# Kernel tuning notes

Hardware: AMD Instinct MI355X
Metric: run time of the kernel (lower is better)

The kernel has to match this reference:

```python
import jax, jax.numpy as jnp
import numpy as np

B, S, D, H, E = 2, 2048, 1024, 4096, 8


def setup_inputs() -> dict:
    key = jax.random.key(0)
    ks = jax.random.split(key, 8)
    sc = lambda *shape: 0.02
    x = jax.random.normal(ks[0], (B, S, D), dtype=jnp.float32)
    gate_w = jax.random.normal(ks[1], (D, E), dtype=jnp.float32) * 0.02
    gate_b = jnp.zeros((E,), dtype=jnp.float32)
    w1 = jax.random.normal(ks[2], (E, D, H), dtype=jnp.float32) * 0.02
    b1 = jnp.zeros((E, H), dtype=jnp.float32)
    w2 = jax.random.normal(ks[3], (E, H, D), dtype=jnp.float32) * 0.02
    b2 = jnp.zeros((E, D), dtype=jnp.float32)
    return {"x": x, "gate_w": gate_w, "gate_b": gate_b,
            "w1": w1, "b1": b1, "w2": w2, "b2": b2}


def reference(x, gate_w, gate_b, w1, b1, w2, b2):
    b, s, d = x.shape
    e = w1.shape[0]
    xf = x.reshape(-1, d)                       # [N, D]
    scores = xf @ gate_w + gate_b               # [N, E]
    # original does topk(k=2) but only uses topk_indices[:, 0] == argmax
    sel = jnp.argmax(scores, axis=-1)           # [N]
    out = jnp.zeros_like(xf)
    for ei in range(e):                         # small fixed expert loop
        h = jax.nn.gelu(xf @ w1[ei] + b1[ei], approximate=False)
        y = h @ w2[ei] + b2[ei]
        out = out + jnp.where((sel == ei)[:, None], y, jnp.zeros((), x.dtype))
    out = out.reshape(b, s, d)
    l_aux = jnp.zeros((), dtype=x.dtype)
    return out, l_aux
```

## Files before the change

### kernel.cpp

```cpp
#include <hip/hip_runtime.h>
#include <math.h>

#define NTOK 4096
#define DDIM 1024
#define HDIM 4096
#define NEXP 8
#define BK 64
#define T0MAX 40
#define T1MAX 72

typedef float f32x4 __attribute__((ext_vector_type(4)));
typedef __bf16 bf16x8 __attribute__((ext_vector_type(8)));
typedef const __attribute__((address_space(1))) void gas_t;
typedef __attribute__((address_space(3))) void las_t;

__device__ __forceinline__ unsigned short f2bf(float f) {
    union { float f; unsigned u; } v; v.f = f;
    unsigned u = v.u;
    return (unsigned short)((u + 0x7fffu + ((u >> 16) & 1u)) >> 16);
}

__device__ __forceinline__ float gelu_f(float v) {
    return 0.5f * v * (1.0f + erff(v * 0.70710678118654752f));
}

__global__ void k_gate(const float* __restrict__ x, const float* __restrict__ gw,
                       const float* __restrict__ gb, unsigned short* __restrict__ xb,
                       int* __restrict__ sel, int* __restrict__ counts) {
    const int wid = threadIdx.x >> 6, lane = threadIdx.x & 63;
    const int tok = blockIdx.x * 4 + wid;
    const float* xr = x + (long)tok * DDIM;
    unsigned short* xbr = xb + (long)tok * DDIM;
    float s[NEXP];
#pragma unroll
    for (int e = 0; e < NEXP; ++e) s[e] = 0.f;
    for (int it = 0; it < DDIM / 64; ++it) {
        const int kk = it * 64 + lane;
        const float xv = xr[kk];
        xbr[kk] = f2bf(xv);
        const float4* g4 = (const float4*)(gw + (long)kk * NEXP);
        const float4 g0 = g4[0], g1 = g4[1];
        s[0] += xv * g0.x; s[1] += xv * g0.y; s[2] += xv * g0.z; s[3] += xv * g0.w;
        s[4] += xv * g1.x; s[5] += xv * g1.y; s[6] += xv * g1.z; s[7] += xv * g1.w;
    }
#pragma unroll
    for (int e = 0; e < NEXP; ++e)
        for (int off = 32; off > 0; off >>= 1)
            s[e] += __shfl_down(s[e], off);
    if (lane == 0) {
        float best = s[0] + gb[0]; int bi = 0;
#pragma unroll
        for (int e = 1; e < NEXP; ++e) {
            const float v = s[e] + gb[e];
            if (v > best) { best = v; bi = e; }
        }
        sel[tok] = bi;
        atomicAdd(&counts[bi], 1);
    }
}

__global__ void k_fill(const int* __restrict__ sel, const int* __restrict__ counts,
                       int* __restrict__ cur, int* __restrict__ offs,
                       int* __restrict__ list, int* __restrict__ t0,
                       int* __restrict__ t1, float* __restrict__ laux) {
    const int t = blockIdx.x * blockDim.x + threadIdx.x;
    if (t < NTOK) {
        const int e = sel[t];
        int off_e = 0;
#pragma unroll
        for (int j = 0; j < NEXP; ++j) off_e += (j < e) ? counts[j] : 0;
        list[off_e + atomicAdd(&cur[e], 1)] = t;
    }
    if (t == 0) {
        int o = 0;
        for (int e = 0; e < NEXP; ++e) { offs[e] = o; o += counts[e]; }
        offs[NEXP] = o;
        int i0 = 0;
        for (int e = 0; e < NEXP; ++e)
            for (int m = 0; m < counts[e]; m += 128) t0[i0++] = (e << 16) | m;
        while (i0 < T0MAX) t0[i0++] = -1;
        int i1 = 0;
        for (int e = 0; e < NEXP; ++e)
            for (int m = 0; m < counts[e]; m += 64) t1[i1++] = (e << 16) | m;
        while (i1 < T1MAX) t1[i1++] = -1;
        laux[0] = 0.f;
    }
}

template<int K, int NC>
__global__ __launch_bounds__(256) void k_cvt_w(const float* __restrict__ W,
                                               unsigned short* __restrict__ Wt) {
    __shared__ unsigned short T[64 * 68];
    const int ktiles = K / 64;
    const int e  = blockIdx.y / ktiles;
    const int k0 = (blockIdx.y % ktiles) * 64;
    const int n0 = blockIdx.x * 64;
    const float* src = W + (long)e * K * NC + (long)k0 * NC + n0;
    const int tid = threadIdx.x;
#pragma unroll
    for (int i = 0; i < 4; ++i) {
        const int idx = tid + i * 256;
        const int k = idx >> 4, c4 = (idx & 15) * 4;
        const float4 v = *(const float4*)(src + (long)k * NC + c4);
        T[(c4 + 0) * 68 + k] = f2bf(v.x);
        T[(c4 + 1) * 68 + k] = f2bf(v.y);
        T[(c4 + 2) * 68 + k] = f2bf(v.z);
        T[(c4 + 3) * 68 + k] = f2bf(v.w);
    }
    __syncthreads();
    unsigned short* dst = Wt + (long)e * NC * K + (long)n0 * K + k0;
#pragma unroll
    for (int i = 0; i < 2; ++i) {
        const int idx = tid + i * 256;
        const int n = idx >> 3, c8 = (idx & 7) * 8;
        *(ushort4*)(dst + (long)n * K + c8)     = *(const ushort4*)&T[n * 68 + c8];
        *(ushort4*)(dst + (long)n * K + c8 + 4) = *(const ushort4*)&T[n * 68 + c8 + 4];
    }
}

template<int MODE, int BM_, int BN_>
__global__ __launch_bounds__(256) void k_gemm(
        const unsigned short* __restrict__ Ain,
        const unsigned short* __restrict__ Wt,
        const float* __restrict__ bias,
        unsigned short* __restrict__ Hout, float* __restrict__ Yout,
        const int* __restrict__ counts, const int* __restrict__ offs,
        const int* __restrict__ list, const int* __restrict__ ttab) {
    static_assert(BM_ % 32 == 0 && BN_ % 32 == 0, "tile");
    constexpr int K  = (MODE == 0) ? DDIM : HDIM;
    constexpr int NC = (MODE == 0) ? HDIM : DDIM;
    constexpr int NT = K / BK;
    constexpr int FM = BM_ / 32;
    constexpr int FN = BN_ / 32;
    constexpr int LA = BM_ / 32;
    constexpr int LB = BN_ / 32;
    constexpr int EP = 136;
    constexpr int STAGE_SH = BM_ * 64 + BN_ * 64;
    constexpr int SH_SZ = (MODE == 0 && BM_ * EP > STAGE_SH) ? BM_ * EP : STAGE_SH;

    const int code = ttab[blockIdx.y];
    if (code < 0) return;
    const int e  = code >> 16;
    const int m0 = code & 0xFFFF;
    const int cnt  = counts[e];
    const int base = offs[e];
    const int n0   = blockIdx.x * BN_;

    __shared__ __align__(16) unsigned short sh[SH_SZ];
    unsigned short* Asb = sh;
    unsigned short* Btb = sh + BM_ * 64;

    const int tid  = threadIdx.x;
    const int lane = tid & 63, wid = tid >> 6;
    const int lr = lane >> 3, lc = lane & 7;
    const int sb = (lc * 16) ^ (lr << 4);

    const unsigned short* pA[LA];
#pragma unroll
    for (int i = 0; i < LA; ++i) {
        const int r = wid * (BM_ / 4) + i * 8 + lr;
        int rr = m0 + r; if (rr >= cnt) rr = cnt - 1;
        const long grow = (MODE == 0) ? (long)list[base + rr] : (long)(base + rr);
        pA[i] = (const unsigned short*)((const char*)(Ain + grow * K) + sb);
    }
    const unsigned short* We = Wt + (long)e * NC * K;
    const unsigned short* pB[LB];
#pragma unroll
    for (int i = 0; i < LB; ++i) {
        const int r = wid * (BN_ / 4) + i * 8 + lr;
        pB[i] = (const unsigned short*)((const char*)(We + (long)(n0 + r) * K) + sb);
    }

    const int wm = (wid >> 1) * (BM_ / 2);
    const int wn = (wid & 1) * 64;
    const int hk = 16 * (lane >> 4);

    const f32x4 zero4 = {0.f, 0.f, 0.f, 0.f};
    f32x4 acc[FM][FN];
#pragma unroll
    for (int i = 0; i < FM; ++i)
#pragma unroll
        for (int j = 0; j < FN; ++j) acc[i][j] = zero4;

    for (int t = 0; t < NT; ++t) {
        __syncthreads();
#pragma unroll
        for (int i = 0; i < LA; ++i)
            __builtin_amdgcn_global_load_lds((gas_t*)(pA[i] + t * 64),
                (las_t*)(Asb + (wid * (BM_ / 4) + i * 8) * 64), 16, 0, 0);
#pragma unroll
        for (int i = 0; i < LB; ++i)
            __builtin_amdgcn_global_load_lds((gas_t*)(pB[i] + t * 64),
                (las_t*)(Btb + (wid * (BN_ / 4) + i * 8) * 64), 16, 0, 0);
        __syncthreads();
#pragma unroll
        for (int kk = 0; kk < BK; kk += 32) {
            bf16x8 a[FM], b[FN];
#pragma unroll
            for (int mf = 0; mf < FM; ++mf) {
                const int r  = wm + mf * 16 + (lane & 15);
                const int kb = (2 * kk + hk) ^ ((r & 7) << 4);
                a[mf] = *(const bf16x8*)((const char*)Asb + r * 128 + kb);
            }
#pragma unroll
            for (int nf = 0; nf < FN; ++nf) {
                const int cc = wn + nf * 16 + (lane & 15);
                const int kb = (2 * kk + hk) ^ ((cc & 7) << 4);
                b[nf] = *(const bf16x8*)((const char*)Btb + cc * 128 + kb);
            }
            __builtin_amdgcn_s_setprio(1);
#pragma unroll
            for (int mf = 0; mf < FM; ++mf)
#pragma unroll
                for (int nf = 0; nf < FN; ++nf)
                    acc[mf][nf] = __builtin_amdgcn_mfma_f32_16x16x32_bf16(
                        a[mf], b[nf], acc[mf][nf], 0, 0, 0);
            __builtin_amdgcn_s_setprio(0);
        }
    }

    if constexpr (MODE == 0) {
        __syncthreads();
#pragma unroll
        for (int nf = 0; nf < FN; ++nf) {
            const int cl = wn + nf * 16 + (lane & 15);
            const float bv = bias[(long)e * NC + n0 + cl];
#pragma unroll
            for (int mf = 0; mf < FM; ++mf) {
#pragma unroll
                for (int ri = 0; ri < 4; ++ri) {
                    const int rl = wm + mf * 16 + (lane >> 4) * 4 + ri;
                    sh[rl * EP + cl] = f2bf(gelu_f(acc[mf][nf][ri] + bv));
                }
            }
        }
        __syncthreads();
        const int row = tid >> 1, ch = (tid & 1) * 64;
        if (m0 + row < cnt) {
            char* dst = (char*)(Hout + (long)(base + m0 + row) * HDIM + n0 + ch);
            const char* srcp = (const char*)sh + row * (EP * 2) + ch * 2;
#pragma unroll
            for (int j = 0; j < 4; ++j) {
                const int4 v0 = *(const int4*)(srcp + j * 32);
                const int4 v1 = *(const int4*)(srcp + j * 32 + 16);
                *(int4*)(dst + j * 32)      = v0;
                *(int4*)(dst + j * 32 + 16) = v1;
            }
        }
    } else {
#pragma unroll
        for (int nf = 0; nf < FN; ++nf) {
            const int coln = n0 + wn + nf * 16 + (lane & 15);
            const float bv = bias[(long)e * NC + coln];
#pragma unroll
            for (int mf = 0; mf < FM; ++mf) {
                const int rb = m0 + wm + mf * 16 + (lane >> 4) * 4;
#pragma unroll
                for (int ri = 0; ri < 4; ++ri) {
                    const int row = rb + ri;
                    if (row < cnt)
                        Yout[(long)list[base + row] * DDIM + coln] = acc[mf][nf][ri] + bv;
                }
            }
        }
    }
}

extern "C" void kernel_launch(void* const* d_in, const int* in_sizes, int n_in,
                              void* d_out, int out_size, void* d_ws, size_t ws_size,
                              hipStream_t stream) {
    const float* x      = (const float*)d_in[0];
    const float* gate_w = (const float*)d_in[1];
    const float* gate_b = (const float*)d_in[2];
    const float* w1     = (const float*)d_in[3];
    const float* b1     = (const float*)d_in[4];
    const float* w2     = (const float*)d_in[5];
    const float* b2     = (const float*)d_in[6];
    float* out = (float*)d_out;

    char* ws = (char*)d_ws;
    int* counts  = (int*)(ws);
    int* cur     = (int*)(ws + 128);
    int* offs    = (int*)(ws + 256);
    int* t0      = (int*)(ws + 512);
    int* t1      = (int*)(ws + 768);
    int* sel     = (int*)(ws + 4096);
    int* list    = (int*)(ws + 20480);
    unsigned short* xb  = (unsigned short*)(ws + 65536);
    unsigned short* Hws = (unsigned short*)(ws + 65536 + 8388608);
    unsigned short* Wtb = (unsigned short*)(ws + 65536 + 8388608 + 33554432);
    const size_t WS_NEEDED = 65536 + 8388608 + 33554432 + 67108864;
    if (ws_size < WS_NEEDED) return;

    hipMemsetAsync(ws, 0, 256, stream);
    k_gate<<<NTOK / 4, 256, 0, stream>>>(x, gate_w, gate_b, xb, sel, counts);
    k_fill<<<(NTOK + 255) / 256, 256, 0, stream>>>(sel, counts, cur, offs, list, t0, t1,
                                                   out + (long)NTOK * DDIM);

    k_cvt_w<DDIM, HDIM><<<dim3(HDIM / 64, NEXP * (DDIM / 64)), 256, 0, stream>>>(w1, Wtb);
    k_gemm<0, 128, 128><<<dim3(HDIM / 128, T0MAX), 256, 0, stream>>>(
        xb, Wtb, b1, Hws, nullptr, counts, offs, list, t0);

    k_cvt_w<HDIM, DDIM><<<dim3(DDIM / 64, NEXP * (HDIM / 64)), 256, 0, stream>>>(w2, Wtb);
    k_gemm<1, 64, 128><<<dim3(DDIM / 128, T1MAX), 256, 0, stream>>>(
        Hws, Wtb, b2, nullptr, out, counts, offs, list, t1);
}
```

Before: 279.8 us.

## Shrink GEMM LDS footprint with two-pass epilogue and smaller second-GEMM tile

The first GEMM's epilogue now stages its GELU output through LDS in two 64-row halves, so shared memory is only as large as the staging buffers rather than BM*136. This lowers LDS use per block and may allow more resident blocks per CU, at the cost of an extra barrier pass. The second GEMM moves from a 64x128 tile to a 64x64 tile, doubling the column-block grid, and the warp column offset is generalised to BN/2 so the smaller tile works.

New measurement: 291.1 us. 1.04x slower.

```diff
diff --git a/kernel.cpp b/kernel.cpp
--- a/kernel.cpp
+++ b/kernel.cpp
@@ -135,8 +135,6 @@
     constexpr int LA = BM_ / 32;
     constexpr int LB = BN_ / 32;
     constexpr int EP = 136;
-    constexpr int STAGE_SH = BM_ * 64 + BN_ * 64;
-    constexpr int SH_SZ = (MODE == 0 && BM_ * EP > STAGE_SH) ? BM_ * EP : STAGE_SH;
 
     const int code = ttab[blockIdx.y];
     if (code < 0) return;
@@ -146,7 +144,7 @@
     const int base = offs[e];
     const int n0   = blockIdx.x * BN_;
 
-    __shared__ __align__(16) unsigned short sh[SH_SZ];
+    __shared__ __align__(16) unsigned short sh[BM_ * 64 + BN_ * 64];
     unsigned short* Asb = sh;
     unsigned short* Btb = sh + BM_ * 64;
 
@@ -172,7 +170,7 @@
     }
 
     const int wm = (wid >> 1) * (BM_ / 2);
-    const int wn = (wid & 1) * 64;
+    const int wn = (wid & 1) * (BN_ / 2);
     const int hk = 16 * (lane >> 4);
 
     const f32x4 zero4 = {0.f, 0.f, 0.f, 0.f};
@@ -220,31 +218,36 @@
     }
 
     if constexpr (MODE == 0) {
-        __syncthreads();
-#pragma unroll
-        for (int nf = 0; nf < FN; ++nf) {
-            const int cl = wn + nf * 16 + (lane & 15);
-            const float bv = bias[(long)e * NC + n0 + cl];
-#pragma unroll
-            for (int mf = 0; mf < FM; ++mf) {
-#pragma unroll
-                for (int ri = 0; ri < 4; ++ri) {
-                    const int rl = wm + mf * 16 + (lane >> 4) * 4 + ri;
-                    sh[rl * EP + cl] = f2bf(gelu_f(acc[mf][nf][ri] + bv));
+        float bvv[FN];
+#pragma unroll
+        for (int nf = 0; nf < FN; ++nf)
+            bvv[nf] = bias[(long)e * NC + n0 + wn + nf * 16 + (lane & 15)];
+#pragma unroll
+        for (int p = 0; p < 2; ++p) {
+            __syncthreads();
+            if ((wid >> 1) == p) {
+#pragma unroll
+                for (int nf = 0; nf < FN; ++nf) {
+                    const int cl = wn + nf * 16 + (lane & 15);
+#pragma unroll
+                    for (int mf = 0; mf < FM; ++mf) {
+#pragma unroll
+                        for (int ri = 0; ri < 4; ++ri) {
+                            const int rl = mf * 16 + (lane >> 4) * 4 + ri;
+                            sh[rl * EP + cl] = f2bf(gelu_f(acc[mf][nf][ri] + bvv[nf]));
+                        }
+                    }
                 }
             }
-        }
-        __syncthreads();
-        const int row = tid >> 1, ch = (tid & 1) * 64;
-        if (m0 + row < cnt) {
-            char* dst = (char*)(Hout + (long)(base + m0 + row) * HDIM + n0 + ch);
-            const char* srcp = (const char*)sh + row * (EP * 2) + ch * 2;
-#pragma unroll
-            for (int j = 0; j < 4; ++j) {
-                const int4 v0 = *(const int4*)(srcp + j * 32);
-                const int4 v1 = *(const int4*)(srcp + j * 32 + 16);
-                *(int4*)(dst + j * 32)      = v0;
-                *(int4*)(dst + j * 32 + 16) = v1;
+            __syncthreads();
+            const int row_l = tid >> 2, q = tid & 3;
+            const int grow = m0 + p * 64 + row_l;
+            if (grow < cnt) {
+                char* dst = (char*)(Hout + (long)(base + grow) * HDIM + n0 + q * 32);
+                const char* srcp = (const char*)sh + row_l * (EP * 2) + q * 64;
+#pragma unroll
+                for (int j = 0; j < 4; ++j)
+                    *(int4*)(dst + j * 16) = *(const int4*)(srcp + j * 16);
             }
         }
     } else {
@@ -302,6 +305,6 @@
         xb, Wtb, b1, Hws, nullptr, counts, offs, list, t0);
 
     k_cvt_w<HDIM, DDIM><<<dim3(DDIM / 64, NEXP * (HDIM / 64)), 256, 0, stream>>>(w2, Wtb);
-    k_gemm<1, 64, 128><<<dim3(DDIM / 128, T1MAX), 256, 0, stream>>>(
+    k_gemm<1, 64, 64><<<dim3(DDIM / 64, T1MAX), 256, 0, stream>>>(
         Hws, Wtb, b2, nullptr, out, counts, offs, list, t1);
 }
```

## Double-buffer GEMM LDS tiles with prefetch two stages ahead; shrink second GEMM tile

Applied to the files above, without the earlier changes.

Each GEMM's shared-memory tile storage is split into two halves. Global-to-LDS loads for tile t+2 are issued right after computing tile t, and a vmcnt wait is placed before each barrier, so memory transfer overlaps with MFMA work instead of stalling at every K step. The second GEMM now uses 64x64 tiles with twice as many column blocks, which changes the warp column offset and adds parallelism on that launch. In exchange the kernel uses twice the LDS, which may reduce occupancy, and correctness depends on the hand-written waitcnt counts matching the number of outstanding loads.

Measured after the change: 285.2 us. No clear change (+1.9%).

```diff
diff --git a/kernel.cpp b/kernel.cpp
--- a/kernel.cpp
+++ b/kernel.cpp
@@ -127,16 +127,16 @@
         const int* __restrict__ counts, const int* __restrict__ offs,
         const int* __restrict__ list, const int* __restrict__ ttab) {
     static_assert(BM_ % 32 == 0 && BN_ % 32 == 0, "tile");
-    constexpr int K  = (MODE == 0) ? DDIM : HDIM;
-    constexpr int NC = (MODE == 0) ? HDIM : DDIM;
-    constexpr int NT = K / BK;
-    constexpr int FM = BM_ / 32;
-    constexpr int FN = BN_ / 32;
-    constexpr int LA = BM_ / 32;
-    constexpr int LB = BN_ / 32;
-    constexpr int EP = 136;
-    constexpr int STAGE_SH = BM_ * 64 + BN_ * 64;
-    constexpr int SH_SZ = (MODE == 0 && BM_ * EP > STAGE_SH) ? BM_ * EP : STAGE_SH;
+    constexpr int K    = (MODE == 0) ? DDIM : HDIM;
+    constexpr int NC   = (MODE == 0) ? HDIM : DDIM;
+    constexpr int NT   = K / BK;
+    constexpr int FM   = BM_ / 32;
+    constexpr int FN   = BN_ / 32;
+    constexpr int LA   = BM_ / 32;
+    constexpr int LB   = BN_ / 32;
+    constexpr int HALF = BM_ * 64 + BN_ * 64;
+    constexpr int EP   = 136;
+    constexpr int SH_SZ = (2 * HALF > BM_ * EP) ? 2 * HALF : BM_ * EP;
 
     const int code = ttab[blockIdx.y];
     if (code < 0) return;
@@ -147,8 +147,6 @@
     const int n0   = blockIdx.x * BN_;
 
     __shared__ __align__(16) unsigned short sh[SH_SZ];
-    unsigned short* Asb = sh;
-    unsigned short* Btb = sh + BM_ * 64;
 
     const int tid  = threadIdx.x;
     const int lane = tid & 63, wid = tid >> 6;
@@ -172,8 +170,18 @@
     }
 
     const int wm = (wid >> 1) * (BM_ / 2);
-    const int wn = (wid & 1) * 64;
+    const int wn = (wid & 1) * (BN_ / 2);
     const int hk = 16 * (lane >> 4);
+
+#define STAGE(t) do { if ((t) < NT) {                                                    \
+    unsigned short* Ad = sh + ((t) & 1) * HALF + (wid * (BM_ / 4)) * 64;                 \
+    unsigned short* Bd = sh + ((t) & 1) * HALF + BM_ * 64 + (wid * (BN_ / 4)) * 64;      \
+    _Pragma("unroll") for (int i = 0; i < LA; ++i)                                       \
+        __builtin_amdgcn_global_load_lds((gas_t*)(pA[i] + (t) * 64),                     \
+            (las_t*)(Ad + i * 512), 16, 0, 0);                                           \
+    _Pragma("unroll") for (int i = 0; i < LB; ++i)                                       \
+        __builtin_amdgcn_global_load_lds((gas_t*)(pB[i] + (t) * 64),                     \
+            (las_t*)(Bd + i * 512), 16, 0, 0); } } while (0)
 
     const f32x4 zero4 = {0.f, 0.f, 0.f, 0.f};
     f32x4 acc[FM][FN];
@@ -182,17 +190,17 @@
 #pragma unroll
         for (int j = 0; j < FN; ++j) acc[i][j] = zero4;
 
+    STAGE(0);
+    STAGE(1);
+
     for (int t = 0; t < NT; ++t) {
-        __syncthreads();
-#pragma unroll
-        for (int i = 0; i < LA; ++i)
-            __builtin_amdgcn_global_load_lds((gas_t*)(pA[i] + t * 64),
-                (las_t*)(Asb + (wid * (BM_ / 4) + i * 8) * 64), 16, 0, 0);
-#pragma unroll
-        for (int i = 0; i < LB; ++i)
-            __builtin_amdgcn_global_load_lds((gas_t*)(pB[i] + t * 64),
-                (las_t*)(Btb + (wid * (BN_ / 4) + i * 8) * 64), 16, 0, 0);
-        __syncthreads();
+        const unsigned short* Ab = sh + (t & 1) * HALF;
+        const unsigned short* Bb = Ab + BM_ * 64;
+        if (t + 1 < NT) { asm volatile("s_waitcnt vmcnt(%0)" :: "n"(LA + LB) : "memory"); }
+        else            { asm volatile("s_waitcnt vmcnt(0)" ::: "memory"); }
+        __builtin_amdgcn_sched_barrier(0);
+        __builtin_amdgcn_s_barrier();
+        __builtin_amdgcn_sched_barrier(0);
 #pragma unroll
         for (int kk = 0; kk < BK; kk += 32) {
             bf16x8 a[FM], b[FN];
@@ -200,13 +208,13 @@
             for (int mf = 0; mf < FM; ++mf) {
                 const int r  = wm + mf * 16 + (lane & 15);
                 const int kb = (2 * kk + hk) ^ ((r & 7) << 4);
-                a[mf] = *(const bf16x8*)((const char*)Asb + r * 128 + kb);
+                a[mf] = *(const bf16x8*)((const char*)Ab + r * 128 + kb);
             }
 #pragma unroll
             for (int nf = 0; nf < FN; ++nf) {
                 const int cc = wn + nf * 16 + (lane & 15);
                 const int kb = (2 * kk + hk) ^ ((cc & 7) << 4);
-                b[nf] = *(const bf16x8*)((const char*)Btb + cc * 128 + kb);
+                b[nf] = *(const bf16x8*)((const char*)Bb + cc * 128 + kb);
             }
             __builtin_amdgcn_s_setprio(1);
 #pragma unroll
@@ -217,10 +225,14 @@
                         a[mf], b[nf], acc[mf][nf], 0, 0, 0);
             __builtin_amdgcn_s_setprio(0);
         }
-    }
+        __builtin_amdgcn_sched_barrier(0);
+        __builtin_amdgcn_s_barrier();
+        __builtin_amdgcn_sched_barrier(0);
+        STAGE(t + 2);
+    }
+#undef STAGE
 
     if constexpr (MODE == 0) {
-        __syncthreads();
 #pragma unroll
         for (int nf = 0; nf < FN; ++nf) {
             const int cl = wn + nf * 16 + (lane & 15);
@@ -302,6 +314,6 @@
         xb, Wtb, b1, Hws, nullptr, counts, offs, list, t0);
 
     k_cvt_w<HDIM, DDIM><<<dim3(DDIM / 64, NEXP * (HDIM / 64)), 256, 0, stream>>>(w2, Wtb);
-    k_gemm<1, 64, 128><<<dim3(DDIM / 128, T1MAX), 256, 0, stream>>>(
+    k_gemm<1, 64, 64><<<dim3(DDIM / 64, T1MAX), 256, 0, stream>>>(
         Hws, Wtb, b2, nullptr, out, counts, offs, list, t1);
 }
```
